# Performance work log

Measured on AMD Instinct MI355X. Metric: run time of the kernel, lower is better.

Reference implementation:

```python
import jax, jax.numpy as jnp
import numpy as np
from jax import lax

T, X, H = 16384, 256, 1024
A_SCALE, A_IDENT = 0.1, 0.9


def setup_inputs() -> dict:
    key = jax.random.key(0)
    k1, k2, k3 = jax.random.split(key, 3)
    x_seq = jax.random.normal(k1, (T, X), dtype=jnp.float32)
    h0 = jnp.zeros((H,), dtype=jnp.float32)
    # orthogonal-like init for A_raw (QR of a gaussian), lecun_normal for B
    g = jax.random.normal(k2, (H, H), dtype=jnp.float32)
    A_raw, _ = jnp.linalg.qr(g)
    B = jax.random.normal(k3, (H, X), dtype=jnp.float32) * (1.0 / np.sqrt(X))
    c = jnp.zeros((H,), dtype=jnp.float32)
    return {"x_seq": x_seq, "h0": h0, "A_raw": A_raw, "B": B, "c": c}


def reference(x_seq, h0, A_raw, B, c):
    # A = a_identity * I + a_scale * A_raw  (computed in setup(), a parameter transform)
    A = A_IDENT * jnp.eye(H, dtype=x_seq.dtype) + A_SCALE * A_raw
    # Precompute input projections for all timesteps as one GEMM: (T,H)
    Bx_c = x_seq @ B.T + c  # B @ x_t + c for every t

    def step(h, bx_t):
        h_new = jnp.tanh(A @ h + bx_t)
        return h_new, h_new

    _, h_all = lax.scan(step, h0, Bx_c)
    return h_all  # (T, H)
```

## Files before the change

kernel.cpp:

```cpp
#include <hip/hip_runtime.h>
#include <cstdint>

#define T_LEN 16384
#define X_DIM 256
#define H_DIM 1024
#define NREP  8
#define SLOT_U32 1024
#define REP_U32  (2 * SLOT_U32)
#define FLAG_OFF (NREP * REP_U32)

typedef unsigned int u32;
typedef u32   u32x4 __attribute__((ext_vector_type(4)));
typedef float f32x4 __attribute__((ext_vector_type(4)));

__device__ __forceinline__ void coh_store4(u32* p, u32x4 v) {
  asm volatile("global_store_dwordx4 %0, %1, off sc0 sc1" :: "v"(p), "v"(v) : "memory");
}
__device__ __forceinline__ void coh_store1(u32* p, u32 v) {
  asm volatile("global_store_dword %0, %1, off sc0 sc1" :: "v"(p), "v"(v) : "memory");
}
__device__ __forceinline__ u32 coh_load1(const u32* p) {
  u32 v;
  asm volatile("global_load_dword %0, %1, off sc0 sc1\n\ts_waitcnt vmcnt(0)"
               : "=v"(v) : "v"(p) : "memory");
  return v;
}
__device__ __forceinline__ void poll_group(const u32* p, u32x4& a, u32x4& b,
                                           u32x4& c, u32x4& d) {
  asm volatile(
      "global_load_dwordx4 %0, %4, off sc0 sc1\n\t"
      "global_load_dwordx4 %1, %4, off offset:16 sc0 sc1\n\t"
      "global_load_dwordx4 %2, %4, off offset:32 sc0 sc1\n\t"
      "global_load_dwordx4 %3, %4, off offset:48 sc0 sc1\n\t"
      "s_waitcnt vmcnt(0)"
      : "=&v"(a), "=&v"(b), "=&v"(c), "=&v"(d) : "v"(p) : "memory");
}

__device__ __forceinline__ float fast_tanh(float x) {
  x = fminf(9.0f, fmaxf(-9.0f, x));
  const float e = __builtin_amdgcn_exp2f(x * 2.8853900817779268f);
  return (e - 1.0f) * __builtin_amdgcn_rcpf(e + 1.0f);
}

__device__ __forceinline__ float dpp_xor1(float x) {
  return __int_as_float(__builtin_amdgcn_update_dpp(0, __float_as_int(x),
                                                    0xB1, 0xF, 0xF, false));
}
__device__ __forceinline__ float dpp_xor2(float x) {
  return __int_as_float(__builtin_amdgcn_update_dpp(0, __float_as_int(x),
                                                    0x4E, 0xF, 0xF, false));
}

__global__ void hinit(const float* __restrict__ h0, u32* __restrict__ ws) {
  const int i = threadIdx.x;
  const f32x4 h = *(const f32x4*)(h0 + i * 4);
  u32x4 v;
  v.x = __float_as_uint(h[0]) & ~3u;
  v.y = __float_as_uint(h[1]) & ~3u;
  v.z = __float_as_uint(h[2]) & ~3u;
  v.w = __float_as_uint(h[3]) & ~3u;
  const int idx = i * 4;
#pragma unroll
  for (int rep = 0; rep < NREP; ++rep)
    coh_store4(ws + (size_t)rep * REP_U32 + idx, v);
  if (i < 2) coh_store1(ws + FLAG_OFF + i, 0u);
}

__global__ __launch_bounds__(256) void gemm_bx(const float* __restrict__ x,
                                               const float* __restrict__ Bm,
                                               const float* __restrict__ c,
                                               float* __restrict__ out) {
  __shared__ float xs[64][68];
  __shared__ float bs[64][68];

  const int tid = threadIdx.x;
  const int t0  = blockIdx.x * 64;
  const int h0  = blockIdx.y * 64;
  const int lr  = tid >> 4;
  const int lc  = tid & 15;

  float acc[4][4] = {};

  for (int kb = 0; kb < X_DIM; kb += 64) {
    const int kk  = (tid & 15) * 4;
    const int tt0 = tid >> 4;
#pragma unroll
    for (int i = 0; i < 4; ++i) {
      const int tt = tt0 + i * 16;
      const f32x4 xv = *(const f32x4*)(x  + (size_t)(t0 + tt) * X_DIM + kb + kk);
      const f32x4 bv = *(const f32x4*)(Bm + (size_t)(h0 + tt) * X_DIM + kb + kk);
#pragma unroll
      for (int q = 0; q < 4; ++q) {
        xs[kk + q][tt] = xv[q];
        bs[kk + q][tt] = bv[q];
      }
    }
    __syncthreads();

#pragma unroll 8
    for (int k = 0; k < 64; ++k) {
      const f32x4 xv = *(const f32x4*)&xs[k][lr * 4];
      const f32x4 bv = *(const f32x4*)&bs[k][lc * 4];
#pragma unroll
      for (int i = 0; i < 4; ++i)
#pragma unroll
        for (int j = 0; j < 4; ++j)
          acc[i][j] = fmaf(xv[i], bv[j], acc[i][j]);
    }
    __syncthreads();
  }

  const f32x4 cv = *(const f32x4*)(c + h0 + lc * 4);
#pragma unroll
  for (int i = 0; i < 4; ++i) {
    f32x4 o;
#pragma unroll
    for (int j = 0; j < 4; ++j) o[j] = acc[i][j] + cv[j];
    *(f32x4*)(out + (size_t)(t0 + lr * 4 + i) * H_DIM + h0 + lc * 4) = o;
  }
}

__global__ __launch_bounds__(256, 1) void rnn_scan(const float* __restrict__ A_raw,
                                                   float* __restrict__ out,
                                                   u32* __restrict__ ws) {
  const int tid = threadIdx.x;

  if (blockIdx.x >= 64) {
    const u32* flag = ws + FLAG_OFF;
    float f0 = 0.f, f1 = 0.f, f2 = 0.f, f3 = 0.f;
    float f4 = 0.f, f5 = 0.f, f6 = 0.f, f7 = 0.f;
    const float m = 1.0000001f, ad = 1e-9f;
    for (int outer = 0; outer < 32768; ++outer) {
      if (coh_load1(flag) != 0u) break;
      for (int i = 0; i < 256; ++i) {
        f0 = fmaf(f0, m, ad); f1 = fmaf(f1, m, ad);
        f2 = fmaf(f2, m, ad); f3 = fmaf(f3, m, ad);
        f4 = fmaf(f4, m, ad); f5 = fmaf(f5, m, ad);
        f6 = fmaf(f6, m, ad); f7 = fmaf(f7, m, ad);
      }
    }
    if (f0 + f1 + f2 + f3 + f4 + f5 + f6 + f7 == 123456.789f && tid == 0)
      coh_store1(ws + FLAG_OFF + 1, 1u);
    return;
  }

  const int lane    = tid & 63;
  const int wv      = tid >> 6;
  const int wg      = blockIdx.x;
  const int gw      = wg * 4 + wv;
  const int rowbase = gw * 4;
  const int r       = lane & 3;
  const int row     = rowbase + r;

  float a[4][16];
#pragma unroll
  for (int rr = 0; rr < 4; ++rr) {
#pragma unroll
    for (int k4 = 0; k4 < 4; ++k4) {
      const f32x4 v = *(const f32x4*)(A_raw + (size_t)(rowbase + rr) * H_DIM +
                                      lane * 16 + k4 * 4);
#pragma unroll
      for (int q = 0; q < 4; ++q) {
        const int col = lane * 16 + k4 * 4 + q;
        a[rr][k4 * 4 + q] = 0.1f * v[q] + (col == rowbase + rr ? 0.9f : 0.0f);
      }
    }
  }
#pragma unroll
  for (int rr = 0; rr < 4; ++rr)
#pragma unroll
    for (int k = 0; k < 16; ++k)
      asm volatile("" : "+v"(a[rr][k]));

  u32* hbuf = ws;
  const u32* ppoll0 = hbuf + (size_t)(gw & (NREP - 1)) * REP_U32 + 16 * lane;
  u32* pub = hbuf + (size_t)(lane >> 2) * REP_U32 + rowbase + r;

  float bx_val = out[(size_t)0 * H_DIM + row];
  float bx_n1  = out[(size_t)1 * H_DIM + row];

  int  dead    = 1 << 20;
  bool timeout = false;

  for (int t = 0; t < T_LEN; ++t) {
    const u32 tag = (u32)(t & 3);
    const u32* p  = ppoll0 + (t & 1) * SLOT_U32;
    u32x4 hA, hB, hC, hD;
    for (;;) {
      poll_group(p, hA, hB, hC, hD);
      const u32 m = (hA.x ^ tag) | (hA.y ^ tag) | (hA.z ^ tag) | (hA.w ^ tag)
                  | (hB.x ^ tag) | (hB.y ^ tag) | (hB.z ^ tag) | (hB.w ^ tag)
                  | (hC.x ^ tag) | (hC.y ^ tag) | (hC.z ^ tag) | (hC.w ^ tag)
                  | (hD.x ^ tag) | (hD.y ^ tag) | (hD.z ^ tag) | (hD.w ^ tag);
      if ((m & 3u) == 0u) break;
      if (--dead == 0) { timeout = true; break; }
    }
    if (__any(timeout)) {
      if (lane == 0) coh_store1(ws + FLAG_OFF, 1u);
      return;
    }

    const int tn2 = (t + 2 < T_LEN) ? t + 2 : t;
    const float bx_n2 = out[(size_t)tn2 * H_DIM + row];

    const f32x4 f0 = __builtin_bit_cast(f32x4, hA);
    const f32x4 f1 = __builtin_bit_cast(f32x4, hB);
    const f32x4 f2 = __builtin_bit_cast(f32x4, hC);
    const f32x4 f3 = __builtin_bit_cast(f32x4, hD);
    float ac0 = 0.f, ac1 = 0.f, ac2 = 0.f, ac3 = 0.f;
#pragma unroll
    for (int j = 0; j < 4; ++j) {
      ac0 = fmaf(a[0][j], f0[j], ac0); ac1 = fmaf(a[1][j], f0[j], ac1);
      ac2 = fmaf(a[2][j], f0[j], ac2); ac3 = fmaf(a[3][j], f0[j], ac3);
    }
#pragma unroll
    for (int j = 0; j < 4; ++j) {
      ac0 = fmaf(a[0][4 + j], f1[j], ac0); ac1 = fmaf(a[1][4 + j], f1[j], ac1);
      ac2 = fmaf(a[2][4 + j], f1[j], ac2); ac3 = fmaf(a[3][4 + j], f1[j], ac3);
    }
#pragma unroll
    for (int j = 0; j < 4; ++j) {
      ac0 = fmaf(a[0][8 + j], f2[j], ac0); ac1 = fmaf(a[1][8 + j], f2[j], ac1);
      ac2 = fmaf(a[2][8 + j], f2[j], ac2); ac3 = fmaf(a[3][8 + j], f2[j], ac3);
    }
#pragma unroll
    for (int j = 0; j < 4; ++j) {
      ac0 = fmaf(a[0][12 + j], f3[j], ac0); ac1 = fmaf(a[1][12 + j], f3[j], ac1);
      ac2 = fmaf(a[2][12 + j], f3[j], ac2); ac3 = fmaf(a[3][12 + j], f3[j], ac3);
    }

    const float lo01 = (lane & 1) ? ac1 : ac0;
    const float ot01 = (lane & 1) ? ac0 : ac1;
    const float lo23 = (lane & 1) ? ac3 : ac2;
    const float ot23 = (lane & 1) ? ac2 : ac3;
    const float p01  = lo01 + dpp_xor1(ot01);
    const float p23  = lo23 + dpp_xor1(ot23);
    const float keep = (lane & 2) ? p23 : p01;
    const float give = (lane & 2) ? p01 : p23;
    float x = keep + dpp_xor2(give);
    x += __shfl_xor(x, 4, 64);
    x += __shfl_xor(x, 8, 64);
    x += __shfl_xor(x, 16, 64);
    x += __shfl_xor(x, 32, 64);

    const float v = fast_tanh(x + bx_val);
    bx_val = bx_n1;
    bx_n1  = bx_n2;

    const u32 nt = (u32)((t + 1) & 3);
    if (lane < 4 * NREP) {
      coh_store1(pub + (size_t)((t + 1) & 1) * SLOT_U32,
                 (__float_as_uint(v) & ~3u) | nt);
    } else if (lane < 4 * NREP + 4) {
      out[(size_t)t * H_DIM + row] = v;
    }
  }

  if (gw == 0 && lane == 0) coh_store1(ws + FLAG_OFF, 1u);
}

extern "C" void kernel_launch(void* const* d_in, const int* in_sizes, int n_in,
                              void* d_out, int out_size, void* d_ws, size_t ws_size,
                              hipStream_t stream) {
  const float* x    = (const float*)d_in[0];
  const float* h0   = (const float*)d_in[1];
  const float* Araw = (const float*)d_in[2];
  const float* B    = (const float*)d_in[3];
  const float* c    = (const float*)d_in[4];
  float* out = (float*)d_out;
  u32* ws    = (u32*)d_ws;

  hinit<<<1, 256, 0, stream>>>(h0, ws);
  dim3 g(T_LEN / 64, H_DIM / 64);
  gemm_bx<<<g, 256, 0, stream>>>(x, B, c, out);
  rnn_scan<<<256, 256, 0, stream>>>(Araw, out, ws);
}
```

Before: 25.01 ms.

## Stream pre-transformed A from workspace each step instead of holding it in registers

Adds an aprep kernel that forms A = 0.9I + 0.1*A_raw once and stores it in the workspace in a per-lane interleaved layout. When the workspace is large enough, the scan kernel reloads A with vector loads every timestep (expected to hit cache) instead of keeping 64 floats per lane in registers. It also drops the launch_bounds occupancy hint of 1 and the register-pinning asm. The aim is to cut register pressure on the latency-bound recurrence, at the cost of 16 extra vector loads per step on the critical path.

```diff
diff --git a/kernel.cpp b/kernel.cpp
--- a/kernel.cpp
+++ b/kernel.cpp
@@ -8,6 +8,8 @@
 #define SLOT_U32 1024
 #define REP_U32  (2 * SLOT_U32)
 #define FLAG_OFF (NREP * REP_U32)
+#define ATR_OFF_U32 32768
+#define WS_NEED ((size_t)ATR_OFF_U32 * 4 + (size_t)H_DIM * H_DIM * 4)
 
 typedef unsigned int u32;
 typedef u32   u32x4 __attribute__((ext_vector_type(4)));
@@ -66,6 +68,26 @@
   if (i < 2) coh_store1(ws + FLAG_OFF + i, 0u);
 }
 
+__global__ __launch_bounds__(256) void aprep(const float* __restrict__ A_raw,
+                                             float* __restrict__ atr) {
+  const int gw   = blockIdx.x;
+  const int lane = threadIdx.x & 63;
+  const int rr   = threadIdx.x >> 6;
+  const int row  = gw * 4 + rr;
+#pragma unroll
+  for (int k4 = 0; k4 < 4; ++k4) {
+    const f32x4 v = *(const f32x4*)(A_raw + (size_t)row * H_DIM +
+                                    lane * 16 + k4 * 4);
+    f32x4 o;
+#pragma unroll
+    for (int q = 0; q < 4; ++q) {
+      const int col = lane * 16 + k4 * 4 + q;
+      o[q] = 0.1f * v[q] + (col == row ? 0.9f : 0.0f);
+    }
+    *(f32x4*)(atr + ((size_t)((gw * 4 + rr) * 4 + k4) * 64 + lane) * 4) = o;
+  }
+}
+
 __global__ __launch_bounds__(256) void gemm_bx(const float* __restrict__ x,
                                                const float* __restrict__ Bm,
                                                const float* __restrict__ c,
@@ -120,9 +142,10 @@
   }
 }
 
-__global__ __launch_bounds__(256, 1) void rnn_scan(const float* __restrict__ A_raw,
-                                                   float* __restrict__ out,
-                                                   u32* __restrict__ ws) {
+template <bool FAST>
+__global__ __launch_bounds__(256) void rnn_scan(const float* __restrict__ A_raw,
+                                                float* __restrict__ out,
+                                                u32* __restrict__ ws) {
   const int tid = threadIdx.x;
 
   if (blockIdx.x >= 64) {
@@ -153,24 +176,22 @@
   const int row     = rowbase + r;
 
   float a[4][16];
-#pragma unroll
-  for (int rr = 0; rr < 4; ++rr) {
-#pragma unroll
-    for (int k4 = 0; k4 < 4; ++k4) {
-      const f32x4 v = *(const f32x4*)(A_raw + (size_t)(rowbase + rr) * H_DIM +
-                                      lane * 16 + k4 * 4);
-#pragma unroll
-      for (int q = 0; q < 4; ++q) {
-        const int col = lane * 16 + k4 * 4 + q;
-        a[rr][k4 * 4 + q] = 0.1f * v[q] + (col == rowbase + rr ? 0.9f : 0.0f);
-      }
-    }
-  }
-#pragma unroll
-  for (int rr = 0; rr < 4; ++rr)
-#pragma unroll
-    for (int k = 0; k < 16; ++k)
-      asm volatile("" : "+v"(a[rr][k]));
+  const float* ab = (const float*)(ws + ATR_OFF_U32) + (size_t)gw * 4096 + lane * 4;
+  if constexpr (!FAST) {
+#pragma unroll
+    for (int rr = 0; rr < 4; ++rr) {
+#pragma unroll
+      for (int k4 = 0; k4 < 4; ++k4) {
+        const f32x4 v = *(const f32x4*)(A_raw + (size_t)(rowbase + rr) * H_DIM +
+                                        lane * 16 + k4 * 4);
+#pragma unroll
+        for (int q = 0; q < 4; ++q) {
+          const int col = lane * 16 + k4 * 4 + q;
+          a[rr][k4 * 4 + q] = 0.1f * v[q] + (col == rowbase + rr ? 0.9f : 0.0f);
+        }
+      }
+    }
+  }
 
   u32* hbuf = ws;
   const u32* ppoll0 = hbuf + (size_t)(gw & (NREP - 1)) * REP_U32 + 16 * lane;
@@ -203,30 +224,39 @@
     const int tn2 = (t + 2 < T_LEN) ? t + 2 : t;
     const float bx_n2 = out[(size_t)tn2 * H_DIM + row];
 
-    const f32x4 f0 = __builtin_bit_cast(f32x4, hA);
-    const f32x4 f1 = __builtin_bit_cast(f32x4, hB);
-    const f32x4 f2 = __builtin_bit_cast(f32x4, hC);
-    const f32x4 f3 = __builtin_bit_cast(f32x4, hD);
+    const f32x4 fh[4] = { __builtin_bit_cast(f32x4, hA),
+                          __builtin_bit_cast(f32x4, hB),
+                          __builtin_bit_cast(f32x4, hC),
+                          __builtin_bit_cast(f32x4, hD) };
     float ac0 = 0.f, ac1 = 0.f, ac2 = 0.f, ac3 = 0.f;
-#pragma unroll
-    for (int j = 0; j < 4; ++j) {
-      ac0 = fmaf(a[0][j], f0[j], ac0); ac1 = fmaf(a[1][j], f0[j], ac1);
-      ac2 = fmaf(a[2][j], f0[j], ac2); ac3 = fmaf(a[3][j], f0[j], ac3);
-    }
-#pragma unroll
-    for (int j = 0; j < 4; ++j) {
-      ac0 = fmaf(a[0][4 + j], f1[j], ac0); ac1 = fmaf(a[1][4 + j], f1[j], ac1);
-      ac2 = fmaf(a[2][4 + j], f1[j], ac2); ac3 = fmaf(a[3][4 + j], f1[j], ac3);
-    }
-#pragma unroll
-    for (int j = 0; j < 4; ++j) {
-      ac0 = fmaf(a[0][8 + j], f2[j], ac0); ac1 = fmaf(a[1][8 + j], f2[j], ac1);
-      ac2 = fmaf(a[2][8 + j], f2[j], ac2); ac3 = fmaf(a[3][8 + j], f2[j], ac3);
-    }
-#pragma unroll
-    for (int j = 0; j < 4; ++j) {
-      ac0 = fmaf(a[0][12 + j], f3[j], ac0); ac1 = fmaf(a[1][12 + j], f3[j], ac1);
-      ac2 = fmaf(a[2][12 + j], f3[j], ac2); ac3 = fmaf(a[3][12 + j], f3[j], ac3);
+    if constexpr (FAST) {
+#pragma unroll
+      for (int k4 = 0; k4 < 4; ++k4) {
+        const f32x4 h4 = fh[k4];
+        const f32x4 a0 = *(const f32x4*)(ab + (0 * 4 + k4) * 256);
+        const f32x4 a1 = *(const f32x4*)(ab + (1 * 4 + k4) * 256);
+        const f32x4 a2 = *(const f32x4*)(ab + (2 * 4 + k4) * 256);
+        const f32x4 a3 = *(const f32x4*)(ab + (3 * 4 + k4) * 256);
+#pragma unroll
+        for (int q = 0; q < 4; ++q) {
+          ac0 = fmaf(a0[q], h4[q], ac0);
+          ac1 = fmaf(a1[q], h4[q], ac1);
+          ac2 = fmaf(a2[q], h4[q], ac2);
+          ac3 = fmaf(a3[q], h4[q], ac3);
+        }
+      }
+    } else {
+#pragma unroll
+      for (int k4 = 0; k4 < 4; ++k4) {
+        const f32x4 h4 = fh[k4];
+#pragma unroll
+        for (int q = 0; q < 4; ++q) {
+          ac0 = fmaf(a[0][k4 * 4 + q], h4[q], ac0);
+          ac1 = fmaf(a[1][k4 * 4 + q], h4[q], ac1);
+          ac2 = fmaf(a[2][k4 * 4 + q], h4[q], ac2);
+          ac3 = fmaf(a[3][k4 * 4 + q], h4[q], ac3);
+        }
+      }
     }
 
     const float lo01 = (lane & 1) ? ac1 : ac0;
@@ -270,8 +300,12 @@
   float* out = (float*)d_out;
   u32* ws    = (u32*)d_ws;
 
+  const bool fast = ws_size >= WS_NEED;
+
   hinit<<<1, 256, 0, stream>>>(h0, ws);
+  if (fast) aprep<<<256, 256, 0, stream>>>(Araw, (float*)(ws + ATR_OFF_U32));
   dim3 g(T_LEN / 64, H_DIM / 64);
   gemm_bx<<<g, 256, 0, stream>>>(x, B, c, out);
-  rnn_scan<<<256, 256, 0, stream>>>(Araw, out, ws);
-}
+  if (fast) rnn_scan<true ><<<256, 256, 0, stream>>>(Araw, out, ws);
+  else      rnn_scan<false><<<256, 256, 0, stream>>>(Araw, out, ws);
+}
```

Measured after the change: 35.88 ms. 43.5% more time.
